# Performance work log

Measured on AMD Instinct MI355X. Metric: run time of the kernel, lower is better.

Reference implementation:

```python
import jax, jax.numpy as jnp
import numpy as np

T, B, S = 12, 65536, 1024       # time steps, total pedestrians, scenes
P = B // S                      # peds per scene (uniform segments)
H_DIM = 64                      # enc_h_dim
D = 4 * H_DIM                   # 256 = concat(h_fwd,h_rev,c_fwd,c_rev)
MLP = 32                        # mlp_dim (obs_enc_feat width)
ZS = 32                         # zS_dim


def setup_inputs() -> dict:
    key = jax.random.key(0)
    ks = jax.random.split(key, 16)
    sc = 1.0 / np.sqrt(H_DIM)
    G = 4 * H_DIM  # gate width (i,f,g,o)
    starts = jnp.arange(S, dtype=jnp.int32) * P
    seq_start_end = jnp.stack([starts, starts + P], axis=1)
    return {
        "last_obs_traj": jax.random.normal(ks[0], (B, 6), jnp.float32),
        "fut_rel_traj": jax.random.normal(ks[1], (T, B, 2), jnp.float32),
        "seq_start_end": seq_start_end,
        "obs_enc_feat": jax.random.normal(ks[2], (B, MLP), jnp.float32),
        "fut_obst": jnp.zeros((T, S, 1), jnp.float32),  # unused by forward
        # initial_h_model / initial_c_model (Linear 6 -> H_DIM)
        "w_h0": jax.random.normal(ks[3], (6, H_DIM), jnp.float32) * sc,
        "b_h0": jnp.zeros((H_DIM,), jnp.float32),
        "w_c0": jax.random.normal(ks[4], (6, H_DIM), jnp.float32) * sc,
        "b_c0": jnp.zeros((H_DIM,), jnp.float32),
        # bidirectional LSTM (input 2, hidden H_DIM), gate order i,f,g,o
        "w_ih_f": jax.random.normal(ks[5], (2, G), jnp.float32) * sc,
        "w_hh_f": jax.random.normal(ks[6], (H_DIM, G), jnp.float32) * sc,
        "b_f": jnp.zeros((G,), jnp.float32),
        "w_ih_r": jax.random.normal(ks[7], (2, G), jnp.float32) * sc,
        "w_hh_r": jax.random.normal(ks[8], (H_DIM, G), jnp.float32) * sc,
        "b_r": jnp.zeros((G,), jnp.float32),
        # fc2: Linear(4h + 4h + mlp_dim -> zS_dim)
        "w_fc2": jax.random.normal(ks[9], (2 * D + MLP, ZS), jnp.float32) * 0.05,
        "b_fc2": jnp.zeros((ZS,), jnp.float32),
    }


def _lstm_scan(xs, h0, c0, w_ih, w_hh, b):
    """Run an LSTM over xs (T,B,in); return final (h, c). Gate order i,f,g,o."""
    def step(carry, x):
        h, c = carry
        z = x @ w_ih + h @ w_hh + b
        i, f, g, o = jnp.split(z, 4, axis=-1)
        c = jax.nn.sigmoid(f) * c + jax.nn.sigmoid(i) * jnp.tanh(g)
        h = jax.nn.sigmoid(o) * jnp.tanh(c)
        return (h, c), None
    (hT, cT), _ = jax.lax.scan(step, (h0, c0), xs)
    return hT, cT


def reference(last_obs_traj, fut_rel_traj, seq_start_end, obs_enc_feat, fut_obst,
              w_h0, b_h0, w_c0, b_c0,
              w_ih_f, w_hh_f, b_f, w_ih_r, w_hh_r, b_r,
              w_fc2, b_fc2):
    # initial states: forward direction from linear maps, reverse direction zeros
    h0_f = last_obs_traj @ w_h0 + b_h0
    c0_f = last_obs_traj @ w_c0 + b_c0
    zeros = jnp.zeros_like(h0_f)

    hf, cf = _lstm_scan(fut_rel_traj, h0_f, c0_f, w_ih_f, w_hh_f, b_f)
    hr, cr = _lstm_scan(fut_rel_traj[::-1], zeros, zeros, w_ih_r, w_hh_r, b_r)

    # torch: state = cat((h_n, c_n), dim=0).permute(1,0,2).reshape(B, 4h)
    final_encoder_h = jnp.concatenate([hf, hr, cf, cr], axis=1)  # (B, 256)

    # per-scene softmax attention pooling: context = softmax(H H^T) @ H
    n_scenes = seq_start_end.shape[0]
    Hs = final_encoder_h.reshape(n_scenes, -1, final_encoder_h.shape[1])  # (S,P,D)
    attn = jax.nn.softmax(jnp.einsum('spd,sqd->spq', Hs, Hs), axis=-1)
    pool_h = jnp.einsum('spq,sqd->spd', attn, Hs).reshape(final_encoder_h.shape)

    dist_fc_input = jnp.concatenate([final_encoder_h, pool_h, obs_enc_feat], axis=1)
    stats = dist_fc_input @ w_fc2 + b_fc2
    return dist_fc_input, stats
```

## Files before the change

### kernel.cpp

```cpp
#include <hip/hip_runtime.h>

#define T_STEPS 12
#define NPED 65536
#define NSCENE 1024
#define PSC 64
#define HID 64
#define DDIM 256
#define DIST 544
#define ZS 32

typedef unsigned int u32;
typedef unsigned short u16;
typedef __attribute__((ext_vector_type(8))) short bf16x8;
typedef __attribute__((ext_vector_type(4))) float f32x4;

__device__ __forceinline__ float u2f(u32 u) { union { u32 i; float f; } v; v.i = u; return v.f; }
__device__ __forceinline__ u32 f2u(float f) { union { float f; u32 i; } v; v.f = f; return v.i; }
__device__ __forceinline__ float bf2f(u16 u) { return u2f(((u32)u) << 16); }
__device__ __forceinline__ u16 f2bf(float f) {
  u32 i = f2u(f);
  return (u16)((i + 0x7fffu + ((i >> 16) & 1u)) >> 16);
}
__device__ __forceinline__ u32 pack2(float a, float b) { return (u32)f2bf(a) | (((u32)f2bf(b)) << 16); }
__device__ __forceinline__ u32 pktrunc(float a, float b) { return (f2u(a) >> 16) | (f2u(b) & 0xffff0000u); }

__device__ __forceinline__ float fsig(float x) { return __builtin_amdgcn_rcpf(1.0f + __expf(-x)); }
__device__ __forceinline__ float ftanh(float x) {
  float e = __expf(fminf(fmaxf(2.0f * x, -80.0f), 80.0f));
  return (e - 1.0f) * __builtin_amdgcn_rcpf(e + 1.0f);
}
__device__ __forceinline__ void unpack8(const uint4 v, float* f) {
  f[0] = u2f(v.x << 16); f[1] = u2f(v.x & 0xffff0000u);
  f[2] = u2f(v.y << 16); f[3] = u2f(v.y & 0xffff0000u);
  f[4] = u2f(v.z << 16); f[5] = u2f(v.z & 0xffff0000u);
  f[6] = u2f(v.w << 16); f[7] = u2f(v.w & 0xffff0000u);
}

__device__ __forceinline__ bool inputs_are_bf16(const u16* probe) {
  const int lane = threadIdx.x & 63;
  const u16 w = probe[2 * lane];
  const u32 e = (w >> 7) & 0xffu;
  const bool ok = (w == 0) || (e >= 96u && e <= 144u);
  return __popcll(__ballot(ok)) >= 48;
}

template<bool FP32>
__device__ __forceinline__ float ld(const void* p, int idx) {
  if (FP32) return ((const float*)p)[idx];
  return bf2f(((const u16*)p)[idx]);
}
template<bool FP32>
__device__ __forceinline__ void ld8(const void* p, size_t idx8, float* f) {
  if (FP32) {
    const float4 a = ((const float4*)p)[idx8 >> 2];
    const float4 b = ((const float4*)p)[(idx8 >> 2) + 1];
    f[0] = a.x; f[1] = a.y; f[2] = a.z; f[3] = a.w;
    f[4] = b.x; f[5] = b.y; f[6] = b.z; f[7] = b.w;
  } else {
    unpack8(((const uint4*)p)[idx8 >> 3], f);
  }
}
template<bool FP32>
__device__ __forceinline__ void ldpair(const void* p, size_t pairidx, float& a, float& b) {
  if (FP32) {
    const float2 v = ((const float2*)p)[pairidx];
    a = v.x; b = v.y;
  } else {
    const u32 xx = ((const u32*)p)[pairidx];
    a = u2f(xx << 16); b = u2f(xx & 0xffff0000u);
  }
}
template<bool FP32>
__device__ __forceinline__ void st8(void* p, size_t idx8, const float* f) {
  if (FP32) {
    float4 a; a.x = f[0]; a.y = f[1]; a.z = f[2]; a.w = f[3];
    float4 b; b.x = f[4]; b.y = f[5]; b.z = f[6]; b.w = f[7];
    ((float4*)p)[idx8 >> 2] = a;
    ((float4*)p)[(idx8 >> 2) + 1] = b;
  } else {
    uint4 pk;
    pk.x = pack2(f[0], f[1]); pk.y = pack2(f[2], f[3]);
    pk.z = pack2(f[4], f[5]); pk.w = pack2(f[6], f[7]);
    ((uint4*)p)[idx8 >> 3] = pk;
  }
}
template<bool FP32>
__device__ __forceinline__ void st4(void* p, size_t idx4, const float4 v) {
  if (FP32) {
    ((float4*)p)[idx4 >> 2] = v;
  } else {
    uint2 pk; pk.x = pack2(v.x, v.y); pk.y = pack2(v.z, v.w);
    *(uint2*)((u16*)p + idx4) = pk;
  }
}

template<bool FP32>
__device__ __forceinline__ void lstm_body(
    const void* __restrict__ last_obs, const void* __restrict__ fut,
    const void* __restrict__ w_h0, const void* __restrict__ b_h0,
    const void* __restrict__ w_c0, const void* __restrict__ b_c0,
    const void* __restrict__ w_ih_f, const void* __restrict__ w_hh_f, const void* __restrict__ b_gf,
    const void* __restrict__ w_ih_r, const void* __restrict__ w_hh_r, const void* __restrict__ b_gr,
    void* __restrict__ outv,
    u16* __restrict__ wTp, u16* __restrict__ wXp, u16* __restrict__ hbp)
{
  const int tid  = threadIdx.x;
  const int wave = tid >> 6;
  const int lane = tid & 63;
  const int l15  = lane & 15;
  const int lhi  = lane >> 4;
  const int ped0 = blockIdx.x * 64 + wave * 16;
  const int xm   = (lane & 7) << 4;
  const int e0   = (lhi * 16) ^ xm;
  const int e1   = (64 + lhi * 16) ^ xm;
  const int foff0 = l15 * 128 + e0;
  const int foff1 = l15 * 128 + e1;
  char* const hw = (char*)hbp + wave * 2048;
  char* const wb = (char*)wTp;
  char* const wxrow = (char*)wXp + l15 * 128;

  float c[16];

  for (int dir = 0; dir < 2; ++dir) {
    const void* whh = dir ? w_hh_r : w_hh_f;
    const void* wih = dir ? w_ih_r : w_ih_f;
    const void* bg  = dir ? b_gr  : b_gf;

    __syncthreads();
    #pragma unroll
    for (int c8 = 0; c8 < 8; ++c8) {
      const int n = tid, k0 = c8 * 8;
      u32 pk[4];
      #pragma unroll
      for (int h = 0; h < 4; ++h) {
        u16 ea, eb;
        if (FP32) {
          ea = f2bf(((const float*)whh)[(k0 + 2 * h) * DDIM + n]);
          eb = f2bf(((const float*)whh)[(k0 + 2 * h + 1) * DDIM + n]);
        } else {
          ea = ((const u16*)whh)[(k0 + 2 * h) * DDIM + n];
          eb = ((const u16*)whh)[(k0 + 2 * h + 1) * DDIM + n];
        }
        pk[h] = (u32)ea | ((u32)eb << 16);
      }
      uint4 v; v.x = pk[0]; v.y = pk[1]; v.z = pk[2]; v.w = pk[3];
      *(uint4*)(wb + n * 128 + ((k0 * 2) ^ ((n & 7) << 4))) = v;
    }
    {
      const int tg2 = tid >> 4, col = tid & 15;
      const float wi0 = ld<FP32>(wih, tg2 * 16 + col);
      const float wi1 = ld<FP32>(wih, DDIM + tg2 * 16 + col);
      const float bb  = ld<FP32>(bg,  tg2 * 16 + col);
      char* const wx = (char*)wXp;
      const int base = (tg2 >> 1) * 2048 + col * 128;
      const int kofs = (tg2 & 1) * 64;
      const int swz  = (col & 7) << 4;
      uint4 v0; v0.x = pack2(wi0, wi1); v0.y = (u32)f2bf(bb); v0.z = 0u; v0.w = 0u;
      uint4 zz; zz.x = 0u; zz.y = 0u; zz.z = 0u; zz.w = 0u;
      *(uint4*)(wx + base + ((kofs +  0) ^ swz)) = v0;
      *(uint4*)(wx + base + ((kofs + 16) ^ swz)) = zz;
      *(uint4*)(wx + base + ((kofs + 32) ^ swz)) = zz;
      *(uint4*)(wx + base + ((kofs + 48) ^ swz)) = zz;
    }

    if (dir == 0) {
      float xo[4][6];
      #pragma unroll
      for (int r = 0; r < 4; ++r)
        #pragma unroll
        for (int k = 0; k < 6; ++k)
          xo[r][k] = ld<FP32>(last_obs, (ped0 + lhi * 4 + r) * 6 + k);
      #pragma unroll
      for (int jj = 0; jj < 4; ++jj) {
        const int j = jj * 16 + l15;
        float wh[6], wc[6];
        #pragma unroll
        for (int k = 0; k < 6; ++k) {
          wh[k] = ld<FP32>(w_h0, k * HID + j);
          wc[k] = ld<FP32>(w_c0, k * HID + j);
        }
        const float bh = ld<FP32>(b_h0, j), bc = ld<FP32>(b_c0, j);
        #pragma unroll
        for (int r = 0; r < 4; ++r) {
          float h0 = bh, c0 = bc;
          #pragma unroll
          for (int k = 0; k < 6; ++k) {
            h0 = fmaf(xo[r][k], wh[k], h0);
            c0 = fmaf(xo[r][k], wc[k], c0);
          }
          c[jj * 4 + r] = c0;
          const int p = lhi * 4 + r;
          *(u16*)(hw + p * 128 + ((j * 2) ^ ((p & 7) << 4))) = f2bf(h0);
        }
      }
    } else {
      #pragma unroll
      for (int jj = 0; jj < 4; ++jj) {
        const int j = jj * 16 + l15;
        #pragma unroll
        for (int r = 0; r < 4; ++r) {
          c[jj * 4 + r] = 0.0f;
          const int p = lhi * 4 + r;
          *(u16*)(hw + p * 128 + ((j * 2) ^ ((p & 7) << 4))) = 0;
        }
      }
    }
    __syncthreads();

    for (int t = 0; t < T_STEPS; ++t) {
      const int tt = dir ? (T_STEPS - 1 - t) : t;
      float xa, xb2;
      ldpair<FP32>(fut, (size_t)tt * NPED + ped0 + l15, xa, xb2);
      union { bf16x8 v; u32 w[4]; } ax;
      ax.w[0] = (lhi == 0) ? pack2(xa, xb2) : 0u;
      ax.w[1] = (lhi == 0) ? 0x00003f80u : 0u;
      ax.w[2] = 0u; ax.w[3] = 0u;

      __asm__ volatile("" ::: "memory");
      const bf16x8 a0 = *(const bf16x8*)(hw + foff0);
      const bf16x8 a1 = *(const bf16x8*)(hw + foff1);

      f32x4 acc[16];
      #pragma unroll
      for (int tg = 0; tg < 16; ++tg) {
        const bf16x8 bx = *(const bf16x8*)(wxrow + (tg >> 1) * 2048 + ((tg & 1) ? e1 : e0));
        const bf16x8 b0 = *(const bf16x8*)(wb + tg * 2048 + foff0);
        const bf16x8 b1 = *(const bf16x8*)(wb + tg * 2048 + foff1);
        f32x4 z = {0.0f, 0.0f, 0.0f, 0.0f};
        z = __builtin_amdgcn_mfma_f32_16x16x32_bf16(ax.v, bx, z, 0, 0, 0);
        z = __builtin_amdgcn_mfma_f32_16x16x32_bf16(a0, b0, z, 0, 0, 0);
        acc[tg] = __builtin_amdgcn_mfma_f32_16x16x32_bf16(a1, b1, z, 0, 0, 0);
      }
      __asm__ volatile("" ::: "memory");

      #pragma unroll
      for (int jj = 0; jj < 4; ++jj) {
        const int j = jj * 16 + l15;
        #pragma unroll
        for (int r = 0; r < 4; ++r) {
          const float ig = fsig(acc[jj][r]);
          const float fg = fsig(acc[jj + 4][r]);
          const float gg = ftanh(acc[jj + 8][r]);
          const float og = fsig(acc[jj + 12][r]);
          const float cn = fmaf(fg, c[jj * 4 + r], ig * gg);
          c[jj * 4 + r] = cn;
          const float hn = og * ftanh(cn);
          const int p = lhi * 4 + r;
          *(u16*)(hw + p * 128 + ((j * 2) ^ ((p & 7) << 4))) = f2bf(hn);
        }
      }
      __asm__ volatile("" ::: "memory");
    }

    __syncthreads();
    float* const tb = (float*)wTp + wave * 1024;
    #pragma unroll
    for (int jj = 0; jj < 4; ++jj)
      #pragma unroll
      for (int r = 0; r < 4; ++r)
        tb[(lhi * 4 + r) * 64 + jj * 16 + l15] = c[jj * 4 + r];
    __asm__ volatile("" ::: "memory");
    #pragma unroll
    for (int r = 0; r < 4; ++r) {
      const int pl = r * 4 + lhi;
      const u32* hp = (const u32*)(hw + pl * 128 + ((l15 * 8) ^ ((pl & 7) << 4)));
      const u32 h01 = hp[0], h23 = hp[1];
      float4 hv;
      hv.x = u2f(h01 << 16); hv.y = u2f(h01 & 0xffff0000u);
      hv.z = u2f(h23 << 16); hv.w = u2f(h23 & 0xffff0000u);
      const float4 cv = *(const float4*)&tb[pl * 64 + l15 * 4];
      const size_t rb = (size_t)(ped0 + pl) * DIST;
      st4<FP32>(outv, rb + (dir ? 64 : 0) + l15 * 4, hv);
      st4<FP32>(outv, rb + 128 + (dir ? 64 : 0) + l15 * 4, cv);
    }
  }
}

__global__ __launch_bounds__(256, 2)
void lstm_kernel(const void* last_obs, const void* fut,
                 const void* w_h0, const void* b_h0,
                 const void* w_c0, const void* b_c0,
                 const void* w_ih_f, const void* w_hh_f, const void* b_gf,
                 const void* w_ih_r, const void* w_hh_r, const void* b_gr,
                 void* outv)
{
  __shared__ __align__(16) u16 wT[DDIM * HID];
  __shared__ __align__(16) u16 wX[8 * 1024];
  __shared__ __align__(16) u16 hb[4][16 * HID];
  if (inputs_are_bf16((const u16*)fut))
    lstm_body<false>(last_obs, fut, w_h0, b_h0, w_c0, b_c0,
                     w_ih_f, w_hh_f, b_gf, w_ih_r, w_hh_r, b_gr, outv, wT, wX, &hb[0][0]);
  else
    lstm_body<true>(last_obs, fut, w_h0, b_h0, w_c0, b_c0,
                    w_ih_f, w_hh_f, b_gf, w_ih_r, w_hh_r, b_gr, outv, wT, wX, &hb[0][0]);
}

template<bool FP32>
__device__ __forceinline__ void pool_body(
    const void* __restrict__ obs, void* __restrict__ outv,
    u16* __restrict__ Hrow, u16* __restrict__ Htr, u16* __restrict__ Pl)
{
  const int tid  = threadIdx.x;
  const int wave = tid >> 6;
  const int lane = tid & 63;
  const int l15  = lane & 15;
  const int lhi  = lane >> 4;
  const int pedbase = blockIdx.x * PSC;
  const int wbase = wave * 16;
  char* const hb = (char*)Hrow;
  char* const tr = (char*)Htr;
  char* const pb = (char*)Pl;
  const int swl = (l15 & 7) << 4;

  if (FP32) {
    const float* ob = (const float*)outv;
    for (int i = tid; i < PSC * 64; i += 256) {
      const int pp = i >> 6, dd = (i & 63) << 2;
      const float4 v = *(const float4*)(ob + (size_t)(pedbase + pp) * DIST + dd);
      uint2 w; w.x = pack2(v.x, v.y); w.y = pack2(v.z, v.w);
      *(uint2*)(hb + pp * 512 + ((2 * dd) ^ ((pp & 7) << 4))) = w;
    }
  } else {
    const u16* ob = (const u16*)outv;
    for (int i = tid; i < PSC * 32; i += 256) {
      const int pp = i >> 5, dd = (i & 31) << 3;
      *(uint4*)(hb + pp * 512 + ((2 * dd) ^ ((pp & 7) << 4))) =
          *(const uint4*)(ob + (size_t)(pedbase + pp) * DIST + dd);
    }
  }
  __syncthreads();

  {
    const int p = tid >> 2, q4 = tid & 3;
    const int swp = (p & 7) << 4;
    #pragma unroll
    for (int j = 0; j < 8; ++j) {
      const int d0 = q4 * 64 + j * 8;
      const uint4 v = *(const uint4*)(hb + p * 512 + ((2 * d0) ^ swp));
      const u16* e = (const u16*)&v;
      #pragma unroll
      for (int jj = 0; jj < 8; ++jj) {
        const int d = d0 + jj;
        *(u16*)(tr + d * 128 + ((2 * p) ^ ((d & 7) << 4))) = e[jj];
      }
    }
  }

  f32x4 acc[4];
  #pragma unroll
  for (int b = 0; b < 4; ++b) acc[b] = (f32x4){0.0f, 0.0f, 0.0f, 0.0f};
  for (int kt = 0; kt < 8; ++kt) {
    const int ko = kt * 64 + lhi * 16;
    const bf16x8 af = *(const bf16x8*)(hb + (wbase + l15) * 512 + (ko ^ swl));
    #pragma unroll
    for (int b = 0; b < 4; ++b) {
      const bf16x8 bf = *(const bf16x8*)(hb + (b * 16 + l15) * 512 + (ko ^ swl));
      acc[b] = __builtin_amdgcn_mfma_f32_16x16x32_bf16(af, bf, acc[b], 0, 0, 0);
    }
  }

  float P[4][4];
  #pragma unroll
  for (int r = 0; r < 4; ++r) {
    float mx = fmaxf(fmaxf(acc[0][r], acc[1][r]), fmaxf(acc[2][r], acc[3][r]));
    mx = fmaxf(mx, __shfl_xor(mx, 1));
    mx = fmaxf(mx, __shfl_xor(mx, 2));
    mx = fmaxf(mx, __shfl_xor(mx, 4));
    mx = fmaxf(mx, __shfl_xor(mx, 8));
    float s = 0.0f;
    #pragma unroll
    for (int b = 0; b < 4; ++b) { P[b][r] = __expf(acc[b][r] - mx); s += P[b][r]; }
    s += __shfl_xor(s, 1); s += __shfl_xor(s, 2);
    s += __shfl_xor(s, 4); s += __shfl_xor(s, 8);
    const float inv = __builtin_amdgcn_rcpf(s);
    #pragma unroll
    for (int b = 0; b < 4; ++b) P[b][r] *= inv;
  }

  #pragma unroll
  for (int b = 0; b < 4; ++b)
    #pragma unroll
    for (int r = 0; r < 4; ++r) {
      const int p = wbase + lhi * 4 + r, q = b * 16 + l15;
      *(u16*)(pb + p * 128 + ((2 * q) ^ ((p & 7) << 4))) = f2bf(P[b][r]);
    }
  __syncthreads();

  float* const stg = (float*)(hb + wave * 8192);
  const bf16x8 pa0 = *(const bf16x8*)(pb + (wbase + l15) * 128 + ((     lhi * 16) ^ swl));
  const bf16x8 pa1 = *(const bf16x8*)(pb + (wbase + l15) * 128 + ((64 + lhi * 16) ^ swl));
  for (int Q = 0; Q < 4; ++Q) {
    f32x4 pv[4];
    #pragma unroll
    for (int n = 0; n < 4; ++n) {
      const int d = (Q * 4 + n) * 16 + l15;
      const int swd = (d & 7) << 4;
      const bf16x8 b0 = *(const bf16x8*)(tr + d * 128 + ((     lhi * 16) ^ swd));
      const bf16x8 b1 = *(const bf16x8*)(tr + d * 128 + ((64 + lhi * 16) ^ swd));
      f32x4 z = {0.0f, 0.0f, 0.0f, 0.0f};
      z = __builtin_amdgcn_mfma_f32_16x16x32_bf16(pa0, b0, z, 0, 0, 0);
      pv[n] = __builtin_amdgcn_mfma_f32_16x16x32_bf16(pa1, b1, z, 0, 0, 0);
    }
    __asm__ volatile("" ::: "memory");
    #pragma unroll
    for (int n = 0; n < 4; ++n)
      #pragma unroll
      for (int r = 0; r < 4; ++r)
        stg[(lhi * 4 + r) * 64 + n * 16 + l15] = pv[n][r];
    __asm__ volatile("" ::: "memory");
    #pragma unroll
    for (int r = 0; r < 4; ++r) {
      const int pl = r * 4 + lhi;
      const float4 cv = *(const float4*)&stg[pl * 64 + l15 * 4];
      st4<FP32>(outv, (size_t)(pedbase + wbase + pl) * DIST + DDIM + Q * 64 + l15 * 4, cv);
    }
    __asm__ volatile("" ::: "memory");
  }

  {
    const int p = tid >> 2, part = tid & 3;
    float ov[8];
    ld8<FP32>(obs, (size_t)(pedbase + p) * ZS + part * 8, ov);
    st8<FP32>(outv, (size_t)(pedbase + p) * DIST + 2 * DDIM + part * 8, ov);
  }
}

__global__ __launch_bounds__(256, 2)
void pool_kernel(const void* fut, const void* obs, void* outv)
{
  __shared__ __align__(16) u16 Hrow[PSC * DDIM];
  __shared__ __align__(16) u16 Htr[DDIM * PSC];
  __shared__ __align__(16) u16 Pl[PSC * PSC];
  if (inputs_are_bf16((const u16*)fut)) pool_body<false>(obs, outv, Hrow, Htr, Pl);
  else                                  pool_body<true>(obs, outv, Hrow, Htr, Pl);
}

template<bool FP32>
__device__ __forceinline__ void fc2_body(
    const void* __restrict__ wfc, const void* __restrict__ bfc,
    void* __restrict__ outv, u16* __restrict__ wl)
{
  const int tid = threadIdx.x;

  if (FP32) {
    const float2* src = (const float2*)wfc;
    for (int i = tid; i < DIST * ZS / 2; i += 256) {
      const float2 v = src[i];
      ((u32*)wl)[i] = pack2(v.x, v.y);
    }
  } else {
    for (int i = tid; i < DIST * ZS / 2; i += 256)
      ((u32*)wl)[i] = ((const u32*)wfc)[i];
  }
  __syncthreads();

  const int p = tid >> 2, part = tid & 3;
  const int ped = blockIdx.x * 64 + p;
  const size_t rowb = (size_t)ped * DIST;

  float acc[8];
  #pragma unroll
  for (int l = 0; l < 8; ++l) acc[l] = 0.0f;

  for (int kc = 0; kc < DIST; kc += 8) {
    float a[8];
    ld8<FP32>(outv, rowb + kc, a);
    #pragma unroll
    for (int l = 0; l < 8; ++l) {
      const float v = a[l];
      float wv[8];
      unpack8(*(const uint4*)&wl[(kc + l) * ZS + part * 8], wv);
      #pragma unroll
      for (int z = 0; z < 8; ++z) acc[z] = fmaf(v, wv[z], acc[z]);
    }
  }
  #pragma unroll
  for (int z = 0; z < 8; ++z) acc[z] += ld<FP32>(bfc, part * 8 + z);
  st8<FP32>(outv, (size_t)NPED * DIST + (size_t)ped * ZS + part * 8, acc);
}

__global__ __launch_bounds__(256, 4)
void fc2_kernel(const void* fut, const void* wfc, const void* bfc, void* outv)
{
  __shared__ __align__(16) u16 wl[DIST * ZS];
  if (inputs_are_bf16((const u16*)fut)) fc2_body<false>(wfc, bfc, outv, wl);
  else                                  fc2_body<true>(wfc, bfc, outv, wl);
}

extern "C" void kernel_launch(void* const* d_in, const int* in_sizes, int n_in,
                              void* d_out, int out_size, void* d_ws, size_t ws_size,
                              hipStream_t stream) {
  const void* last_obs = d_in[0];
  const void* fut      = d_in[1];
  const void* obs      = d_in[3];
  const void* w_h0  = d_in[5];
  const void* b_h0  = d_in[6];
  const void* w_c0  = d_in[7];
  const void* b_c0  = d_in[8];
  const void* w_ih_f = d_in[9];
  const void* w_hh_f = d_in[10];
  const void* b_f    = d_in[11];
  const void* w_ih_r = d_in[12];
  const void* w_hh_r = d_in[13];
  const void* b_r    = d_in[14];
  const void* w_fc2  = d_in[15];
  const void* b_fc2  = d_in[16];

  lstm_kernel<<<dim3(NPED / 64), dim3(256), 0, stream>>>(
      last_obs, fut, w_h0, b_h0, w_c0, b_c0,
      w_ih_f, w_hh_f, b_f, w_ih_r, w_hh_r, b_r, d_out);
  pool_kernel<<<dim3(NSCENE), dim3(256), 0, stream>>>(fut, obs, d_out);
  fc2_kernel<<<dim3(NPED / 64), dim3(256), 0, stream>>>(fut, w_fc2, b_fc2, d_out);
}
```

Baseline: 425.7 us.

## Fuse fc2 projection into pool kernel using bf16 MFMA

Removes the separate fc2 kernel and computes the stats projection at the end of the pooling kernel. Each wave multiplies its 16 rows of the 544-wide concatenated input by a bf16 copy of w_fc2 held in swizzled LDS, using 16x16x32 MFMA instead of scalar FMAs. This drops one launch and part of the global re-read of the concatenated rows, at the cost of an extra LDS weight fill per block and a reuse of the pooling LDS region. The rows are read back from global memory right after the same block wrote them, which relies on intra-block visibility after a barrier.

```diff
diff --git a/kernel.cpp b/kernel.cpp
--- a/kernel.cpp
+++ b/kernel.cpp
@@ -22,7 +22,6 @@
   return (u16)((i + 0x7fffu + ((i >> 16) & 1u)) >> 16);
 }
 __device__ __forceinline__ u32 pack2(float a, float b) { return (u32)f2bf(a) | (((u32)f2bf(b)) << 16); }
-__device__ __forceinline__ u32 pktrunc(float a, float b) { return (f2u(a) >> 16) | (f2u(b) & 0xffff0000u); }
 
 __device__ __forceinline__ float fsig(float x) { return __builtin_amdgcn_rcpf(1.0f + __expf(-x)); }
 __device__ __forceinline__ float ftanh(float x) {
@@ -297,8 +296,9 @@
 
 template<bool FP32>
 __device__ __forceinline__ void pool_body(
-    const void* __restrict__ obs, void* __restrict__ outv,
-    u16* __restrict__ Hrow, u16* __restrict__ Htr, u16* __restrict__ Pl)
+    const void* __restrict__ obs, const void* __restrict__ wfc,
+    const void* __restrict__ bfc, void* __restrict__ outv,
+    u16* __restrict__ Hrow, u16* __restrict__ Breg)
 {
   const int tid  = threadIdx.x;
   const int wave = tid >> 6;
@@ -308,8 +308,8 @@
   const int pedbase = blockIdx.x * PSC;
   const int wbase = wave * 16;
   char* const hb = (char*)Hrow;
-  char* const tr = (char*)Htr;
-  char* const pb = (char*)Pl;
+  char* const tr = (char*)Breg;
+  char* const pb = (char*)Breg + 32768;
   const int swl = (l15 & 7) << 4;
 
   if (FP32) {
@@ -423,68 +423,63 @@
     ld8<FP32>(obs, (size_t)(pedbase + p) * ZS + part * 8, ov);
     st8<FP32>(outv, (size_t)(pedbase + p) * DIST + 2 * DDIM + part * 8, ov);
   }
+
+  __syncthreads();
+
+  for (int i = tid; i < DIST * ZS; i += 256) {
+    const int k = i >> 5, z = i & 31;
+    const u16 w = FP32 ? f2bf(((const float*)wfc)[i]) : ((const u16*)wfc)[i];
+    *(u16*)(tr + (k >> 5) * 2048 + z * 64 + ((2 * (k & 31)) ^ ((z & 3) << 4))) = w;
+  }
+  __syncthreads();
+
+  {
+    const size_t rowb = (size_t)(pedbase + wbase + l15) * DIST;
+    f32x4 s0 = {0.0f, 0.0f, 0.0f, 0.0f}, s1 = {0.0f, 0.0f, 0.0f, 0.0f};
+    const int bofs = (lhi * 16) ^ ((l15 & 3) << 4);
+    for (int kt = 0; kt < 17; ++kt) {
+      const int kd = kt * 32 + lhi * 8;
+      union { bf16x8 v; uint4 u; } af;
+      if (FP32) {
+        const float4 a = *(const float4*)((const float*)outv + rowb + kd);
+        const float4 b = *(const float4*)((const float*)outv + rowb + kd + 4);
+        af.u.x = pack2(a.x, a.y); af.u.y = pack2(a.z, a.w);
+        af.u.z = pack2(b.x, b.y); af.u.w = pack2(b.z, b.w);
+      } else {
+        af.u = *(const uint4*)((const u16*)outv + rowb + kd);
+      }
+      const char* wfb = tr + kt * 2048;
+      const bf16x8 b0 = *(const bf16x8*)(wfb + (l15     ) * 64 + bofs);
+      const bf16x8 b1 = *(const bf16x8*)(wfb + (l15 + 16) * 64 + bofs);
+      s0 = __builtin_amdgcn_mfma_f32_16x16x32_bf16(af.v, b0, s0, 0, 0, 0);
+      s1 = __builtin_amdgcn_mfma_f32_16x16x32_bf16(af.v, b1, s1, 0, 0, 0);
+    }
+    const float bb0 = ld<FP32>(bfc, l15), bb1 = ld<FP32>(bfc, 16 + l15);
+    __asm__ volatile("" ::: "memory");
+    #pragma unroll
+    for (int r = 0; r < 4; ++r) {
+      stg[(lhi * 4 + r) * 32 + l15     ] = s0[r] + bb0;
+      stg[(lhi * 4 + r) * 32 + l15 + 16] = s1[r] + bb1;
+    }
+    __asm__ volatile("" ::: "memory");
+    #pragma unroll
+    for (int s = 0; s < 2; ++s) {
+      const int idx = lane * 2 + s;
+      const int pl = idx >> 3, q4 = idx & 7;
+      const float4 v = *(const float4*)&stg[pl * 32 + q4 * 4];
+      st4<FP32>(outv, (size_t)NPED * DIST + (size_t)(pedbase + wbase + pl) * ZS + q4 * 4, v);
+    }
+  }
 }
 
 __global__ __launch_bounds__(256, 2)
-void pool_kernel(const void* fut, const void* obs, void* outv)
+void pool_kernel(const void* fut, const void* obs, const void* wfc,
+                 const void* bfc, void* outv)
 {
   __shared__ __align__(16) u16 Hrow[PSC * DDIM];
-  __shared__ __align__(16) u16 Htr[DDIM * PSC];
-  __shared__ __align__(16) u16 Pl[PSC * PSC];
-  if (inputs_are_bf16((const u16*)fut)) pool_body<false>(obs, outv, Hrow, Htr, Pl);
-  else                                  pool_body<true>(obs, outv, Hrow, Htr, Pl);
-}
-
-template<bool FP32>
-__device__ __forceinline__ void fc2_body(
-    const void* __restrict__ wfc, const void* __restrict__ bfc,
-    void* __restrict__ outv, u16* __restrict__ wl)
-{
-  const int tid = threadIdx.x;
-
-  if (FP32) {
-    const float2* src = (const float2*)wfc;
-    for (int i = tid; i < DIST * ZS / 2; i += 256) {
-      const float2 v = src[i];
-      ((u32*)wl)[i] = pack2(v.x, v.y);
-    }
-  } else {
-    for (int i = tid; i < DIST * ZS / 2; i += 256)
-      ((u32*)wl)[i] = ((const u32*)wfc)[i];
-  }
-  __syncthreads();
-
-  const int p = tid >> 2, part = tid & 3;
-  const int ped = blockIdx.x * 64 + p;
-  const size_t rowb = (size_t)ped * DIST;
-
-  float acc[8];
-  #pragma unroll
-  for (int l = 0; l < 8; ++l) acc[l] = 0.0f;
-
-  for (int kc = 0; kc < DIST; kc += 8) {
-    float a[8];
-    ld8<FP32>(outv, rowb + kc, a);
-    #pragma unroll
-    for (int l = 0; l < 8; ++l) {
-      const float v = a[l];
-      float wv[8];
-      unpack8(*(const uint4*)&wl[(kc + l) * ZS + part * 8], wv);
-      #pragma unroll
-      for (int z = 0; z < 8; ++z) acc[z] = fmaf(v, wv[z], acc[z]);
-    }
-  }
-  #pragma unroll
-  for (int z = 0; z < 8; ++z) acc[z] += ld<FP32>(bfc, part * 8 + z);
-  st8<FP32>(outv, (size_t)NPED * DIST + (size_t)ped * ZS + part * 8, acc);
-}
-
-__global__ __launch_bounds__(256, 4)
-void fc2_kernel(const void* fut, const void* wfc, const void* bfc, void* outv)
-{
-  __shared__ __align__(16) u16 wl[DIST * ZS];
-  if (inputs_are_bf16((const u16*)fut)) fc2_body<false>(wfc, bfc, outv, wl);
-  else                                  fc2_body<true>(wfc, bfc, outv, wl);
+  __shared__ __align__(16) u16 Breg[20480];
+  if (inputs_are_bf16((const u16*)fut)) pool_body<false>(obs, wfc, bfc, outv, Hrow, Breg);
+  else                                  pool_body<true>(obs, wfc, bfc, outv, Hrow, Breg);
 }
 
 extern "C" void kernel_launch(void* const* d_in, const int* in_sizes, int n_in,
@@ -509,6 +504,5 @@
   lstm_kernel<<<dim3(NPED / 64), dim3(256), 0, stream>>>(
       last_obs, fut, w_h0, b_h0, w_c0, b_c0,
       w_ih_f, w_hh_f, b_f, w_ih_r, w_hh_r, b_r, d_out);
-  pool_kernel<<<dim3(NSCENE), dim3(256), 0, stream>>>(fut, obs, d_out);
-  fc2_kernel<<<dim3(NPED / 64), dim3(256), 0, stream>>>(fut, w_fc2, b_fc2, d_out);
-}
+  pool_kernel<<<dim3(NSCENE), dim3(256), 0, stream>>>(fut, obs, w_fc2, b_fc2, d_out);
+}
```

After: 402.5 us. 1.06x faster.
